# Performance work log

Hardware: AMD Instinct MI355X
Metric: run time of the kernel (lower is better)

Reference implementation:

```python
import jax, jax.numpy as jnp
import numpy as np

B, C, H, W = 4, 32, 128, 256
EPS = 1e-5  # BatchNorm eps


def _conv1x1_bn(x, w, b, gamma, beta, mean, var):
    # x: [B,C,H,W]; 1x1 conv == channel matmul, fused with eval-mode BatchNorm
    y = jnp.einsum('bchw,oc->bohw', x, w) + b[None, :, None, None]
    scale = gamma / jnp.sqrt(var + EPS)
    shift = beta - mean * scale
    return y * scale[None, :, None, None] + shift[None, :, None, None]


def setup_inputs() -> dict:
    key = jax.random.key(0)
    ks = jax.random.split(key, 15)
    d = {
        'x_left': jax.random.normal(ks[0], (B, C, H, W), jnp.float32),
        'x_right': jax.random.normal(ks[1], (B, C, H, W), jnp.float32),
        'cost': jax.random.normal(ks[2], (2, B, H, W, W), jnp.float32),
        'q_w': jax.random.normal(ks[3], (C, C), jnp.float32),
        'q_b': jax.random.normal(ks[4], (C,), jnp.float32),
        'q_gamma': jax.random.uniform(ks[5], (C,), jnp.float32),
        'q_beta': jax.random.normal(ks[6], (C,), jnp.float32),
        'q_mean': jax.random.normal(ks[7], (C,), jnp.float32),
        'q_var': jax.random.uniform(ks[8], (C,), jnp.float32),
        'k_w': jax.random.normal(ks[9], (C, C), jnp.float32),
        'k_b': jax.random.normal(ks[10], (C,), jnp.float32),
        'k_gamma': jax.random.uniform(ks[11], (C,), jnp.float32),
        'k_beta': jax.random.normal(ks[12], (C,), jnp.float32),
        'k_mean': jax.random.normal(ks[13], (C,), jnp.float32),
        'k_var': jax.random.uniform(ks[14], (C,), jnp.float32),
    }
    return d


def reference(x_left, x_right, cost, q_w, q_b, q_gamma, q_beta, q_mean, q_var,
              k_w, k_b, k_gamma, k_beta, k_mean, k_var):
    b, c, h, w = x_left.shape
    cr = w // 3  # clamped_range

    # band masks: right2left keeps 0 <= i-j < cr (lower band); left2right keeps 0 <= j-i < cr
    idx = jnp.arange(w)
    diff = idx[:, None] - idx[None, :]  # [W,W] = i - j
    low_band = ((diff >= 0) & (diff < cr)).astype(x_left.dtype)
    up_band = low_band.T

    # right-to-left: Q from left, K from right
    q_l = jnp.transpose(_conv1x1_bn(x_left, q_w, q_b, q_gamma, q_beta, q_mean, q_var), (0, 2, 3, 1))   # [B,H,W,C]
    k_r = jnp.transpose(_conv1x1_bn(x_right, k_w, k_b, k_gamma, k_beta, k_mean, k_var), (0, 2, 3, 1))  # [B,H,W,C]
    s_r2l = jnp.einsum('bhic,bhjc->bhij', q_l, k_r) / c  # [B,H,W,W]
    cost_r2l = s_r2l * low_band + cost[0]

    # left-to-right: Q from right, K from left
    q_r = jnp.transpose(_conv1x1_bn(x_right, q_w, q_b, q_gamma, q_beta, q_mean, q_var), (0, 2, 3, 1))
    k_l = jnp.transpose(_conv1x1_bn(x_left, k_w, k_b, k_gamma, k_beta, k_mean, k_var), (0, 2, 3, 1))
    s_l2r = jnp.einsum('bhic,bhjc->bhij', q_r, k_l) / c
    cost_l2r = s_l2r * up_band + cost[1]

    # original returns (x_left + fea_left, x_right + fea_right, (r2l, l2r)) with fea == x
    return (x_left * 2.0, x_right * 2.0, cost_r2l, cost_l2r)
```

## Files before the change

kernel.cpp:

```cpp
#include <hip/hip_runtime.h>

#define BB 4
#define CC 32
#define HH 128
#define WW 256
#define CR 85
#define EPSF 1e-5f

#define O1_OFF 4194304
#define O2_OFF 8388608
#define COST1 33554432

typedef __attribute__((ext_vector_type(8))) short bf16x8;
typedef __attribute__((ext_vector_type(4))) float f32x4;
typedef __attribute__((ext_vector_type(4))) float f4v;

#define ARR (512 * 256 * 32)
#define WS_Q(side) ((side) * ARR)
#define WS_K(side) (2 * ARR + (side) * ARR)
#define WS_NEEDED (4ull * ARR * 2ull)

static __device__ __forceinline__ unsigned short f2bf(float f) {
    unsigned u = __float_as_uint(f);
    unsigned r = (u + 0x7FFFu + ((u >> 16) & 1u)) >> 16;
    return (unsigned short)r;
}

__global__ __launch_bounds__(256, 4)
void proj_kernel(const float* __restrict__ x_left, const float* __restrict__ x_right,
                 const float* __restrict__ q_w, const float* __restrict__ q_b,
                 const float* __restrict__ q_gamma, const float* __restrict__ q_beta,
                 const float* __restrict__ q_mean, const float* __restrict__ q_var,
                 const float* __restrict__ k_w, const float* __restrict__ k_b,
                 const float* __restrict__ k_gamma, const float* __restrict__ k_beta,
                 const float* __restrict__ k_mean, const float* __restrict__ k_var,
                 float* __restrict__ out, unsigned short* __restrict__ ws)
{
    __shared__ float wq[CC][CC];
    __shared__ float wk[CC][CC];
    __shared__ float bq[CC], bk[CC], sq[CC], sk[CC];

    const int t    = threadIdx.x;
    const int side = blockIdx.x >> 9;
    const int bh   = blockIdx.x & 511;

    if (t < CC) {
        float qs = q_gamma[t] * rsqrtf(q_var[t] + EPSF);
        float ks = k_gamma[t] * rsqrtf(k_var[t] + EPSF);
        sq[t] = qs; sk[t] = ks;
        bq[t] = q_b[t] * qs + q_beta[t] - q_mean[t] * qs;
        bk[t] = k_b[t] * ks + k_beta[t] - k_mean[t] * ks;
    }
    __syncthreads();
    for (int r = t; r < CC * CC; r += 256) {
        int o = r >> 5, c = r & 31;
        wq[c][o] = q_w[r] * sq[o];
        wk[c][o] = k_w[r] * sk[o];
    }
    __syncthreads();

    float q[CC], k[CC];
    #pragma unroll
    for (int o = 0; o < CC; ++o) { q[o] = bq[o]; k[o] = bk[o]; }

    const float* x = side ? x_right : x_left;
    const int b = bh >> 7, h = bh & 127;
    const int xbase = (b * CC * HH + h) * WW + t;
    float* outx = out + side * O1_OFF;

    #pragma unroll 4
    for (int c = 0; c < CC; ++c) {
        int idx = xbase + c * (HH * WW);
        float xv = __builtin_nontemporal_load(x + idx);
        __builtin_nontemporal_store(2.0f * xv, outx + idx);
        #pragma unroll
        for (int o = 0; o < CC; ++o) {
            q[o] += xv * wq[c][o];
            k[o] += xv * wk[c][o];
        }
    }

    unsigned short* qdst = ws + WS_Q(side) + (bh * WW + t) * CC;
    unsigned short* kdst = ws + WS_K(side) + (bh * WW + t) * CC;
    #pragma unroll
    for (int g = 0; g < 4; ++g) {
        uint4 vq, vk;
        vq.x = f2bf(q[8*g+0]) | ((unsigned)f2bf(q[8*g+1]) << 16);
        vq.y = f2bf(q[8*g+2]) | ((unsigned)f2bf(q[8*g+3]) << 16);
        vq.z = f2bf(q[8*g+4]) | ((unsigned)f2bf(q[8*g+5]) << 16);
        vq.w = f2bf(q[8*g+6]) | ((unsigned)f2bf(q[8*g+7]) << 16);
        vk.x = f2bf(k[8*g+0]) | ((unsigned)f2bf(k[8*g+1]) << 16);
        vk.y = f2bf(k[8*g+2]) | ((unsigned)f2bf(k[8*g+3]) << 16);
        vk.z = f2bf(k[8*g+4]) | ((unsigned)f2bf(k[8*g+5]) << 16);
        vk.w = f2bf(k[8*g+6]) | ((unsigned)f2bf(k[8*g+7]) << 16);
        ((uint4*)qdst)[g] = vq;
        ((uint4*)kdst)[g] = vk;
    }
}

__global__ __launch_bounds__(256, 5)
void score_kernel(const float* __restrict__ cost, const unsigned short* __restrict__ ws,
                  float* __restrict__ out)
{
    __shared__ float Sb[32 * 132];

    const int bx   = (blockIdx.x & 7) * 1024 + (blockIdx.x >> 3);
    const int tile = bx & 7;
    const int bh   = (bx >> 3) & 511;
    const int dir  = bx >> 12;
    const int i0   = tile * 32;
    const int wbase = dir ? i0 : (i0 - 96);

    const unsigned short* qsrc = ws + (dir ? WS_Q(1) : WS_Q(0)) + bh * WW * CC;
    const unsigned short* ksrc = ws + (dir ? WS_K(0) : WS_K(1)) + bh * WW * CC;
    const float* csrc = cost + (size_t)dir * COST1 + (size_t)bh * (WW * WW);
    float* odst = out + O2_OFF + (size_t)dir * COST1 + (size_t)bh * (WW * WW);

    const int t = threadIdx.x;
    const int rowlane = t >> 6;
    const int c4 = 4 * (t & 63);

    f4v vbuf[8];
    #pragma unroll
    for (int p = 0; p < 8; ++p) {
        int rl = 4 * p + rowlane;
        vbuf[p] = __builtin_nontemporal_load((const f4v*)(csrc + (i0 + rl) * WW + c4));
    }

    const int w = t >> 6, lane = t & 63;
    const int quad = lane >> 4, l16 = lane & 15;

    bf16x8 qf[2], kf[2];
    #pragma unroll
    for (int mt = 0; mt < 2; ++mt)
        qf[mt] = *(const bf16x8*)(qsrc + (i0 + 16 * mt + l16) * CC + quad * 8);
    #pragma unroll
    for (int nt = 0; nt < 2; ++nt) {
        int col = wbase + 32 * w + 16 * nt + l16;
        bf16x8 kv = {};
        if (col >= 0 && col < WW)
            kv = *(const bf16x8*)(ksrc + col * CC + quad * 8);
        kf[nt] = kv;
    }

    f32x4 acc[2][2] = {};
    #pragma unroll
    for (int mt = 0; mt < 2; ++mt)
        #pragma unroll
        for (int nt = 0; nt < 2; ++nt)
            acc[mt][nt] = __builtin_amdgcn_mfma_f32_16x16x32_bf16(
                qf[mt], kf[nt], acc[mt][nt], 0, 0, 0);

    #pragma unroll
    for (int mt = 0; mt < 2; ++mt)
        #pragma unroll
        for (int nt = 0; nt < 2; ++nt) {
            int cl = 32 * w + 16 * nt + l16;
            #pragma unroll
            for (int r = 0; r < 4; ++r) {
                int row = 16 * mt + quad * 4 + r;
                Sb[row * 132 + cl] = acc[mt][nt][r];
            }
        }
    __syncthreads();

    const float inv32 = 1.0f / 32.0f;
    const int lc = c4 - wbase;
    const bool inwin = (lc >= 0 && lc < 128);

    #pragma unroll
    for (int p = 0; p < 8; ++p) {
        int rl = 4 * p + rowlane;
        int i = i0 + rl;
        f4v v = vbuf[p];
        if (inwin) {
            const f4v s = *(const f4v*)(Sb + rl * 132 + lc);
            int d0 = dir ? (c4 + 0 - i) : (i - c4 - 0);
            int d1 = dir ? (c4 + 1 - i) : (i - c4 - 1);
            int d2 = dir ? (c4 + 2 - i) : (i - c4 - 2);
            int d3 = dir ? (c4 + 3 - i) : (i - c4 - 3);
            if (d0 >= 0 && d0 < CR) v[0] += s[0] * inv32;
            if (d1 >= 0 && d1 < CR) v[1] += s[1] * inv32;
            if (d2 >= 0 && d2 < CR) v[2] += s[2] * inv32;
            if (d3 >= 0 && d3 < CR) v[3] += s[3] * inv32;
        }
        __builtin_nontemporal_store(v, (f4v*)(odst + (size_t)i * WW + c4));
    }
}

__global__ __launch_bounds__(256, 2)
void pab_fused(const float* __restrict__ x_left, const float* __restrict__ x_right,
               const float* __restrict__ cost,
               const float* __restrict__ q_w, const float* __restrict__ q_b,
               const float* __restrict__ q_gamma, const float* __restrict__ q_beta,
               const float* __restrict__ q_mean, const float* __restrict__ q_var,
               const float* __restrict__ k_w, const float* __restrict__ k_b,
               const float* __restrict__ k_gamma, const float* __restrict__ k_beta,
               const float* __restrict__ k_mean, const float* __restrict__ k_var,
               float* __restrict__ out)
{
    __shared__ float qwt[CC][CC];
    __shared__ float kwt[CC][CC];
    __shared__ float qbf[CC], kbf[CC], qsc[CC], ksc[CC];
    __shared__ float Qls[WW][CC];
    __shared__ float Qrs[WW][CC];

    const int t   = threadIdx.x;
    const int bid = blockIdx.x;
    const int b   = bid >> 7;
    const int h   = bid & 127;

    if (t < CC) {
        float qs = q_gamma[t] * rsqrtf(q_var[t] + EPSF);
        float ks = k_gamma[t] * rsqrtf(k_var[t] + EPSF);
        qsc[t] = qs; ksc[t] = ks;
        qbf[t] = q_b[t] * qs + q_beta[t] - q_mean[t] * qs;
        kbf[t] = k_b[t] * ks + k_beta[t] - k_mean[t] * ks;
    }
    __syncthreads();
    for (int r = t; r < CC * CC; r += 256) {
        int o = r >> 5, c = r & 31;
        qwt[c][o] = q_w[r] * qsc[o];
        kwt[c][o] = k_w[r] * ksc[o];
    }
    __syncthreads();

    float ql[CC], qr[CC], kl[CC], kr[CC];
    #pragma unroll
    for (int o = 0; o < CC; ++o) {
        float qb0 = qbf[o], kb0 = kbf[o];
        ql[o] = qb0; qr[o] = qb0; kl[o] = kb0; kr[o] = kb0;
    }
    const int xbase = (b * CC * HH + h) * WW + t;
    #pragma unroll 4
    for (int c = 0; c < CC; ++c) {
        int idx = xbase + c * (HH * WW);
        float xl = x_left[idx];
        float xr = x_right[idx];
        out[idx]          = 2.0f * xl;
        out[O1_OFF + idx] = 2.0f * xr;
        #pragma unroll
        for (int o = 0; o < CC; ++o) {
            float qw = qwt[c][o];
            float kw = kwt[c][o];
            ql[o] += xl * qw;
            kl[o] += xl * kw;
            qr[o] += xr * qw;
            kr[o] += xr * kw;
        }
    }
    #pragma unroll
    for (int o = 0; o < CC; o += 4) {
        *(float4*)&Qls[t][o] = make_float4(ql[o], ql[o+1], ql[o+2], ql[o+3]);
        *(float4*)&Qrs[t][o] = make_float4(qr[o], qr[o+1], qr[o+2], qr[o+3]);
    }
    __syncthreads();

    const int rowbase = bid * (WW * WW) + t;
    const float* __restrict__ c0 = cost + rowbase;
    const float* __restrict__ c1 = cost + COST1 + rowbase;
    float* __restrict__ o2 = out + O2_OFF + rowbase;
    float* __restrict__ o3 = out + O2_OFF + COST1 + rowbase;

    #pragma unroll 2
    for (int i = 0; i < WW; ++i) {
        float v0 = c0[i * WW];
        float v1 = c1[i * WW];
        int d = i - t;
        if (d >= 0 && d < CR) {
            float s = 0.f;
            #pragma unroll
            for (int o = 0; o < CC; o += 4) {
                float4 q = *(const float4*)&Qls[i][o];
                s += q.x * kr[o] + q.y * kr[o+1] + q.z * kr[o+2] + q.w * kr[o+3];
            }
            v0 += s * (1.0f / 32.0f);
        }
        if (d <= 0 && d > -CR) {
            float s = 0.f;
            #pragma unroll
            for (int o = 0; o < CC; o += 4) {
                float4 q = *(const float4*)&Qrs[i][o];
                s += q.x * kl[o] + q.y * kl[o+1] + q.z * kl[o+2] + q.w * kl[o+3];
            }
            v1 += s * (1.0f / 32.0f);
        }
        o2[i * WW] = v0;
        o3[i * WW] = v1;
    }
}

extern "C" void kernel_launch(void* const* d_in, const int* in_sizes, int n_in,
                              void* d_out, int out_size, void* d_ws, size_t ws_size,
                              hipStream_t stream) {
    const float* x_left  = (const float*)d_in[0];
    const float* x_right = (const float*)d_in[1];
    const float* cost    = (const float*)d_in[2];
    const float* q_w     = (const float*)d_in[3];
    const float* q_b     = (const float*)d_in[4];
    const float* q_gamma = (const float*)d_in[5];
    const float* q_beta  = (const float*)d_in[6];
    const float* q_mean  = (const float*)d_in[7];
    const float* q_var   = (const float*)d_in[8];
    const float* k_w     = (const float*)d_in[9];
    const float* k_b     = (const float*)d_in[10];
    const float* k_gamma = (const float*)d_in[11];
    const float* k_beta  = (const float*)d_in[12];
    const float* k_mean  = (const float*)d_in[13];
    const float* k_var   = (const float*)d_in[14];
    float* out = (float*)d_out;

    if (ws_size >= WS_NEEDED) {
        unsigned short* ws = (unsigned short*)d_ws;
        proj_kernel<<<dim3(1024), dim3(256), 0, stream>>>(
            x_left, x_right,
            q_w, q_b, q_gamma, q_beta, q_mean, q_var,
            k_w, k_b, k_gamma, k_beta, k_mean, k_var,
            out, ws);
        score_kernel<<<dim3(8192), dim3(256), 0, stream>>>(cost, ws, out);
    } else {
        pab_fused<<<dim3(BB * HH), dim3(256), 0, stream>>>(
            x_left, x_right, cost,
            q_w, q_b, q_gamma, q_beta, q_mean, q_var,
            k_w, k_b, k_gamma, k_beta, k_mean, k_var,
            out);
    }
}
```

Measured before the change: 547.3 us.

## Fuse projection and score kernels into one per-row kernel with LDS Q/K

Replaces the separate projection kernel and workspace-based score kernel with a single kernel per (direction, batch, row). It computes bf16 Q and K into shared memory and then loops over eight row tiles doing MFMA scores plus the banded cost add. This removes the workspace write/read and one launch. In exchange it recomputes the projections per direction, reads x twice, and reduces parallelism to 1024 blocks with serial tile loops and extra barriers.

```diff
diff --git a/kernel.cpp b/kernel.cpp
--- a/kernel.cpp
+++ b/kernel.cpp
@@ -15,278 +15,180 @@
 typedef __attribute__((ext_vector_type(4))) float f32x4;
 typedef __attribute__((ext_vector_type(4))) float f4v;
 
-#define ARR (512 * 256 * 32)
-#define WS_Q(side) ((side) * ARR)
-#define WS_K(side) (2 * ARR + (side) * ARR)
-#define WS_NEEDED (4ull * ARR * 2ull)
-
 static __device__ __forceinline__ unsigned short f2bf(float f) {
     unsigned u = __float_as_uint(f);
     unsigned r = (u + 0x7FFFu + ((u >> 16) & 1u)) >> 16;
     return (unsigned short)r;
 }
 
-__global__ __launch_bounds__(256, 4)
-void proj_kernel(const float* __restrict__ x_left, const float* __restrict__ x_right,
-                 const float* __restrict__ q_w, const float* __restrict__ q_b,
-                 const float* __restrict__ q_gamma, const float* __restrict__ q_beta,
-                 const float* __restrict__ q_mean, const float* __restrict__ q_var,
-                 const float* __restrict__ k_w, const float* __restrict__ k_b,
-                 const float* __restrict__ k_gamma, const float* __restrict__ k_beta,
-                 const float* __restrict__ k_mean, const float* __restrict__ k_var,
-                 float* __restrict__ out, unsigned short* __restrict__ ws)
+__global__ __launch_bounds__(256, 3)
+void pab_fused_one(const float* __restrict__ x_left, const float* __restrict__ x_right,
+                   const float* __restrict__ cost,
+                   const float* __restrict__ q_w, const float* __restrict__ q_b,
+                   const float* __restrict__ q_gamma, const float* __restrict__ q_beta,
+                   const float* __restrict__ q_mean, const float* __restrict__ q_var,
+                   const float* __restrict__ k_w, const float* __restrict__ k_b,
+                   const float* __restrict__ k_gamma, const float* __restrict__ k_beta,
+                   const float* __restrict__ k_mean, const float* __restrict__ k_var,
+                   float* __restrict__ out)
 {
-    __shared__ float wq[CC][CC];
-    __shared__ float wk[CC][CC];
-    __shared__ float bq[CC], bk[CC], sq[CC], sk[CC];
-
-    const int t    = threadIdx.x;
-    const int side = blockIdx.x >> 9;
-    const int bh   = blockIdx.x & 511;
+    __shared__ unsigned short Qs[WW * CC];
+    __shared__ unsigned short Ks[WW * CC];
+    __shared__ char smem[32 * 132 * 4];
+    float* Sb = (float*)smem;
+    float (*wqs)[CC] = (float(*)[CC])smem;
+    float (*wks)[CC] = (float(*)[CC])(smem + 4096);
+    float* bqs = (float*)(smem + 8192);
+    float* bks = (float*)(smem + 8320);
+    float* sqs = (float*)(smem + 8448);
+    float* sks = (float*)(smem + 8576);
+
+    const int t   = threadIdx.x;
+    const int dir = blockIdx.x >> 9;
+    const int bh  = blockIdx.x & 511;
+    const int b = bh >> 7, h = bh & 127;
 
     if (t < CC) {
-        float qs = q_gamma[t] * rsqrtf(q_var[t] + EPSF);
-        float ks = k_gamma[t] * rsqrtf(k_var[t] + EPSF);
-        sq[t] = qs; sk[t] = ks;
-        bq[t] = q_b[t] * qs + q_beta[t] - q_mean[t] * qs;
-        bk[t] = k_b[t] * ks + k_beta[t] - k_mean[t] * ks;
+        float qs_ = q_gamma[t] * rsqrtf(q_var[t] + EPSF);
+        float ks_ = k_gamma[t] * rsqrtf(k_var[t] + EPSF);
+        sqs[t] = qs_; sks[t] = ks_;
+        bqs[t] = q_b[t] * qs_ + q_beta[t] - q_mean[t] * qs_;
+        bks[t] = k_b[t] * ks_ + k_beta[t] - k_mean[t] * ks_;
     }
     __syncthreads();
     for (int r = t; r < CC * CC; r += 256) {
         int o = r >> 5, c = r & 31;
-        wq[c][o] = q_w[r] * sq[o];
-        wk[c][o] = k_w[r] * sk[o];
+        wqs[c][o] = q_w[r] * sqs[o];
+        wks[c][o] = k_w[r] * sks[o];
     }
     __syncthreads();
 
-    float q[CC], k[CC];
-    #pragma unroll
-    for (int o = 0; o < CC; ++o) { q[o] = bq[o]; k[o] = bk[o]; }
-
-    const float* x = side ? x_right : x_left;
-    const int b = bh >> 7, h = bh & 127;
+    const float* xq = dir ? x_right : x_left;
+    const float* xk = dir ? x_left  : x_right;
+    float* outq = out + (dir ? O1_OFF : 0);
     const int xbase = (b * CC * HH + h) * WW + t;
-    float* outx = out + side * O1_OFF;
-
-    #pragma unroll 4
-    for (int c = 0; c < CC; ++c) {
-        int idx = xbase + c * (HH * WW);
-        float xv = __builtin_nontemporal_load(x + idx);
-        __builtin_nontemporal_store(2.0f * xv, outx + idx);
-        #pragma unroll
-        for (int o = 0; o < CC; ++o) {
-            q[o] += xv * wq[c][o];
-            k[o] += xv * wk[c][o];
-        }
-    }
-
-    unsigned short* qdst = ws + WS_Q(side) + (bh * WW + t) * CC;
-    unsigned short* kdst = ws + WS_K(side) + (bh * WW + t) * CC;
-    #pragma unroll
-    for (int g = 0; g < 4; ++g) {
-        uint4 vq, vk;
-        vq.x = f2bf(q[8*g+0]) | ((unsigned)f2bf(q[8*g+1]) << 16);
-        vq.y = f2bf(q[8*g+2]) | ((unsigned)f2bf(q[8*g+3]) << 16);
-        vq.z = f2bf(q[8*g+4]) | ((unsigned)f2bf(q[8*g+5]) << 16);
-        vq.w = f2bf(q[8*g+6]) | ((unsigned)f2bf(q[8*g+7]) << 16);
-        vk.x = f2bf(k[8*g+0]) | ((unsigned)f2bf(k[8*g+1]) << 16);
-        vk.y = f2bf(k[8*g+2]) | ((unsigned)f2bf(k[8*g+3]) << 16);
-        vk.z = f2bf(k[8*g+4]) | ((unsigned)f2bf(k[8*g+5]) << 16);
-        vk.w = f2bf(k[8*g+6]) | ((unsigned)f2bf(k[8*g+7]) << 16);
-        ((uint4*)qdst)[g] = vq;
-        ((uint4*)kdst)[g] = vk;
-    }
-}
-
-__global__ __launch_bounds__(256, 5)
-void score_kernel(const float* __restrict__ cost, const unsigned short* __restrict__ ws,
-                  float* __restrict__ out)
-{
-    __shared__ float Sb[32 * 132];
-
-    const int bx   = (blockIdx.x & 7) * 1024 + (blockIdx.x >> 3);
-    const int tile = bx & 7;
-    const int bh   = (bx >> 3) & 511;
-    const int dir  = bx >> 12;
-    const int i0   = tile * 32;
-    const int wbase = dir ? i0 : (i0 - 96);
-
-    const unsigned short* qsrc = ws + (dir ? WS_Q(1) : WS_Q(0)) + bh * WW * CC;
-    const unsigned short* ksrc = ws + (dir ? WS_K(0) : WS_K(1)) + bh * WW * CC;
+
+    {
+        float q[CC];
+        #pragma unroll
+        for (int o = 0; o < CC; ++o) q[o] = bqs[o];
+        #pragma unroll 4
+        for (int c = 0; c < CC; ++c) {
+            int idx = xbase + c * (HH * WW);
+            float xv = xq[idx];
+            __builtin_nontemporal_store(2.0f * xv, outq + idx);
+            #pragma unroll
+            for (int o = 0; o < CC; ++o) q[o] += xv * wqs[c][o];
+        }
+        unsigned short* qdst = Qs + t * CC;
+        #pragma unroll
+        for (int g = 0; g < 4; ++g) {
+            uint4 v;
+            v.x = f2bf(q[8*g+0]) | ((unsigned)f2bf(q[8*g+1]) << 16);
+            v.y = f2bf(q[8*g+2]) | ((unsigned)f2bf(q[8*g+3]) << 16);
+            v.z = f2bf(q[8*g+4]) | ((unsigned)f2bf(q[8*g+5]) << 16);
+            v.w = f2bf(q[8*g+6]) | ((unsigned)f2bf(q[8*g+7]) << 16);
+            ((uint4*)qdst)[g] = v;
+        }
+    }
+    {
+        float k[CC];
+        #pragma unroll
+        for (int o = 0; o < CC; ++o) k[o] = bks[o];
+        #pragma unroll 4
+        for (int c = 0; c < CC; ++c) {
+            float xv = xk[xbase + c * (HH * WW)];
+            #pragma unroll
+            for (int o = 0; o < CC; ++o) k[o] += xv * wks[c][o];
+        }
+        unsigned short* kdst = Ks + t * CC;
+        #pragma unroll
+        for (int g = 0; g < 4; ++g) {
+            uint4 v;
+            v.x = f2bf(k[8*g+0]) | ((unsigned)f2bf(k[8*g+1]) << 16);
+            v.y = f2bf(k[8*g+2]) | ((unsigned)f2bf(k[8*g+3]) << 16);
+            v.z = f2bf(k[8*g+4]) | ((unsigned)f2bf(k[8*g+5]) << 16);
+            v.w = f2bf(k[8*g+6]) | ((unsigned)f2bf(k[8*g+7]) << 16);
+            ((uint4*)kdst)[g] = v;
+        }
+    }
+    __syncthreads();
+
     const float* csrc = cost + (size_t)dir * COST1 + (size_t)bh * (WW * WW);
     float* odst = out + O2_OFF + (size_t)dir * COST1 + (size_t)bh * (WW * WW);
-
-    const int t = threadIdx.x;
     const int rowlane = t >> 6;
     const int c4 = 4 * (t & 63);
-
-    f4v vbuf[8];
-    #pragma unroll
-    for (int p = 0; p < 8; ++p) {
-        int rl = 4 * p + rowlane;
-        vbuf[p] = __builtin_nontemporal_load((const f4v*)(csrc + (i0 + rl) * WW + c4));
-    }
-
     const int w = t >> 6, lane = t & 63;
     const int quad = lane >> 4, l16 = lane & 15;
-
-    bf16x8 qf[2], kf[2];
-    #pragma unroll
-    for (int mt = 0; mt < 2; ++mt)
-        qf[mt] = *(const bf16x8*)(qsrc + (i0 + 16 * mt + l16) * CC + quad * 8);
-    #pragma unroll
-    for (int nt = 0; nt < 2; ++nt) {
-        int col = wbase + 32 * w + 16 * nt + l16;
-        bf16x8 kv = {};
-        if (col >= 0 && col < WW)
-            kv = *(const bf16x8*)(ksrc + col * CC + quad * 8);
-        kf[nt] = kv;
-    }
-
-    f32x4 acc[2][2] = {};
-    #pragma unroll
-    for (int mt = 0; mt < 2; ++mt)
-        #pragma unroll
-        for (int nt = 0; nt < 2; ++nt)
-            acc[mt][nt] = __builtin_amdgcn_mfma_f32_16x16x32_bf16(
-                qf[mt], kf[nt], acc[mt][nt], 0, 0, 0);
-
-    #pragma unroll
-    for (int mt = 0; mt < 2; ++mt)
+    const float inv32 = 1.0f / 32.0f;
+
+    for (int tile = 0; tile < 8; ++tile) {
+        const int i0 = tile * 32;
+        const int wbase = dir ? i0 : (i0 - 96);
+
+        f4v vbuf[8];
+        #pragma unroll
+        for (int p = 0; p < 8; ++p) {
+            int rl = 4 * p + rowlane;
+            vbuf[p] = __builtin_nontemporal_load((const f4v*)(csrc + (i0 + rl) * WW + c4));
+        }
+
+        bf16x8 qf[2], kf[2];
+        #pragma unroll
+        for (int mt = 0; mt < 2; ++mt)
+            qf[mt] = *(const bf16x8*)(Qs + (i0 + 16 * mt + l16) * CC + quad * 8);
         #pragma unroll
         for (int nt = 0; nt < 2; ++nt) {
-            int cl = 32 * w + 16 * nt + l16;
-            #pragma unroll
-            for (int r = 0; r < 4; ++r) {
-                int row = 16 * mt + quad * 4 + r;
-                Sb[row * 132 + cl] = acc[mt][nt][r];
+            int col = wbase + 32 * w + 16 * nt + l16;
+            bf16x8 kv = {};
+            if (col >= 0 && col < WW)
+                kv = *(const bf16x8*)(Ks + col * CC + quad * 8);
+            kf[nt] = kv;
+        }
+
+        f32x4 acc[2][2] = {};
+        #pragma unroll
+        for (int mt = 0; mt < 2; ++mt)
+            #pragma unroll
+            for (int nt = 0; nt < 2; ++nt)
+                acc[mt][nt] = __builtin_amdgcn_mfma_f32_16x16x32_bf16(
+                    qf[mt], kf[nt], acc[mt][nt], 0, 0, 0);
+
+        __syncthreads();
+
+        #pragma unroll
+        for (int mt = 0; mt < 2; ++mt)
+            #pragma unroll
+            for (int nt = 0; nt < 2; ++nt) {
+                int cl = 32 * w + 16 * nt + l16;
+                #pragma unroll
+                for (int r = 0; r < 4; ++r) {
+                    int row = 16 * mt + quad * 4 + r;
+                    Sb[row * 132 + cl] = acc[mt][nt][r];
+                }
             }
-        }
-    __syncthreads();
-
-    const float inv32 = 1.0f / 32.0f;
-    const int lc = c4 - wbase;
-    const bool inwin = (lc >= 0 && lc < 128);
-
-    #pragma unroll
-    for (int p = 0; p < 8; ++p) {
-        int rl = 4 * p + rowlane;
-        int i = i0 + rl;
-        f4v v = vbuf[p];
-        if (inwin) {
-            const f4v s = *(const f4v*)(Sb + rl * 132 + lc);
-            int d0 = dir ? (c4 + 0 - i) : (i - c4 - 0);
-            int d1 = dir ? (c4 + 1 - i) : (i - c4 - 1);
-            int d2 = dir ? (c4 + 2 - i) : (i - c4 - 2);
-            int d3 = dir ? (c4 + 3 - i) : (i - c4 - 3);
-            if (d0 >= 0 && d0 < CR) v[0] += s[0] * inv32;
-            if (d1 >= 0 && d1 < CR) v[1] += s[1] * inv32;
-            if (d2 >= 0 && d2 < CR) v[2] += s[2] * inv32;
-            if (d3 >= 0 && d3 < CR) v[3] += s[3] * inv32;
-        }
-        __builtin_nontemporal_store(v, (f4v*)(odst + (size_t)i * WW + c4));
-    }
-}
-
-__global__ __launch_bounds__(256, 2)
-void pab_fused(const float* __restrict__ x_left, const float* __restrict__ x_right,
-               const float* __restrict__ cost,
-               const float* __restrict__ q_w, const float* __restrict__ q_b,
-               const float* __restrict__ q_gamma, const float* __restrict__ q_beta,
-               const float* __restrict__ q_mean, const float* __restrict__ q_var,
-               const float* __restrict__ k_w, const float* __restrict__ k_b,
-               const float* __restrict__ k_gamma, const float* __restrict__ k_beta,
-               const float* __restrict__ k_mean, const float* __restrict__ k_var,
-               float* __restrict__ out)
-{
-    __shared__ float qwt[CC][CC];
-    __shared__ float kwt[CC][CC];
-    __shared__ float qbf[CC], kbf[CC], qsc[CC], ksc[CC];
-    __shared__ float Qls[WW][CC];
-    __shared__ float Qrs[WW][CC];
-
-    const int t   = threadIdx.x;
-    const int bid = blockIdx.x;
-    const int b   = bid >> 7;
-    const int h   = bid & 127;
-
-    if (t < CC) {
-        float qs = q_gamma[t] * rsqrtf(q_var[t] + EPSF);
-        float ks = k_gamma[t] * rsqrtf(k_var[t] + EPSF);
-        qsc[t] = qs; ksc[t] = ks;
-        qbf[t] = q_b[t] * qs + q_beta[t] - q_mean[t] * qs;
-        kbf[t] = k_b[t] * ks + k_beta[t] - k_mean[t] * ks;
-    }
-    __syncthreads();
-    for (int r = t; r < CC * CC; r += 256) {
-        int o = r >> 5, c = r & 31;
-        qwt[c][o] = q_w[r] * qsc[o];
-        kwt[c][o] = k_w[r] * ksc[o];
-    }
-    __syncthreads();
-
-    float ql[CC], qr[CC], kl[CC], kr[CC];
-    #pragma unroll
-    for (int o = 0; o < CC; ++o) {
-        float qb0 = qbf[o], kb0 = kbf[o];
-        ql[o] = qb0; qr[o] = qb0; kl[o] = kb0; kr[o] = kb0;
-    }
-    const int xbase = (b * CC * HH + h) * WW + t;
-    #pragma unroll 4
-    for (int c = 0; c < CC; ++c) {
-        int idx = xbase + c * (HH * WW);
-        float xl = x_left[idx];
-        float xr = x_right[idx];
-        out[idx]          = 2.0f * xl;
-        out[O1_OFF + idx] = 2.0f * xr;
-        #pragma unroll
-        for (int o = 0; o < CC; ++o) {
-            float qw = qwt[c][o];
-            float kw = kwt[c][o];
-            ql[o] += xl * qw;
-            kl[o] += xl * kw;
-            qr[o] += xr * qw;
-            kr[o] += xr * kw;
-        }
-    }
-    #pragma unroll
-    for (int o = 0; o < CC; o += 4) {
-        *(float4*)&Qls[t][o] = make_float4(ql[o], ql[o+1], ql[o+2], ql[o+3]);
-        *(float4*)&Qrs[t][o] = make_float4(qr[o], qr[o+1], qr[o+2], qr[o+3]);
-    }
-    __syncthreads();
-
-    const int rowbase = bid * (WW * WW) + t;
-    const float* __restrict__ c0 = cost + rowbase;
-    const float* __restrict__ c1 = cost + COST1 + rowbase;
-    float* __restrict__ o2 = out + O2_OFF + rowbase;
-    float* __restrict__ o3 = out + O2_OFF + COST1 + rowbase;
-
-    #pragma unroll 2
-    for (int i = 0; i < WW; ++i) {
-        float v0 = c0[i * WW];
-        float v1 = c1[i * WW];
-        int d = i - t;
-        if (d >= 0 && d < CR) {
-            float s = 0.f;
-            #pragma unroll
-            for (int o = 0; o < CC; o += 4) {
-                float4 q = *(const float4*)&Qls[i][o];
-                s += q.x * kr[o] + q.y * kr[o+1] + q.z * kr[o+2] + q.w * kr[o+3];
+        __syncthreads();
+
+        const int lc = c4 - wbase;
+        const bool inwin = (lc >= 0 && lc < 128);
+        #pragma unroll
+        for (int p = 0; p < 8; ++p) {
+            int rl = 4 * p + rowlane;
+            int i = i0 + rl;
+            f4v v = vbuf[p];
+            if (inwin) {
+                const f4v s = *(const f4v*)(Sb + rl * 132 + lc);
+                int d0 = dir ? (c4 + 0 - i) : (i - c4 - 0);
+                int d1 = dir ? (c4 + 1 - i) : (i - c4 - 1);
+                int d2 = dir ? (c4 + 2 - i) : (i - c4 - 2);
+                int d3 = dir ? (c4 + 3 - i) : (i - c4 - 3);
+                if (d0 >= 0 && d0 < CR) v[0] += s[0] * inv32;
+                if (d1 >= 0 && d1 < CR) v[1] += s[1] * inv32;
+                if (d2 >= 0 && d2 < CR) v[2] += s[2] * inv32;
+                if (d3 >= 0 && d3 < CR) v[3] += s[3] * inv32;
             }
-            v0 += s * (1.0f / 32.0f);
-        }
-        if (d <= 0 && d > -CR) {
-            float s = 0.f;
-            #pragma unroll
-            for (int o = 0; o < CC; o += 4) {
-                float4 q = *(const float4*)&Qrs[i][o];
-                s += q.x * kl[o] + q.y * kl[o+1] + q.z * kl[o+2] + q.w * kl[o+3];
-            }
-            v1 += s * (1.0f / 32.0f);
-        }
-        o2[i * WW] = v0;
-        o3[i * WW] = v1;
+            __builtin_nontemporal_store(v, (f4v*)(odst + (size_t)i * WW + c4));
+        }
     }
 }
 
@@ -310,19 +212,9 @@
     const float* k_var   = (const float*)d_in[14];
     float* out = (float*)d_out;
 
-    if (ws_size >= WS_NEEDED) {
-        unsigned short* ws = (unsigned short*)d_ws;
-        proj_kernel<<<dim3(1024), dim3(256), 0, stream>>>(
-            x_left, x_right,
-            q_w, q_b, q_gamma, q_beta, q_mean, q_var,
-            k_w, k_b, k_gamma, k_beta, k_mean, k_var,
-            out, ws);
-        score_kernel<<<dim3(8192), dim3(256), 0, stream>>>(cost, ws, out);
-    } else {
-        pab_fused<<<dim3(BB * HH), dim3(256), 0, stream>>>(
-            x_left, x_right, cost,
-            q_w, q_b, q_gamma, q_beta, q_mean, q_var,
-            k_w, k_b, k_gamma, k_beta, k_mean, k_var,
-            out);
-    }
+    pab_fused_one<<<dim3(1024), dim3(256), 0, stream>>>(
+        x_left, x_right, cost,
+        q_w, q_b, q_gamma, q_beta, q_mean, q_var,
+        k_w, k_b, k_gamma, k_beta, k_mean, k_var,
+        out);
 }
```

Measured after the change: 531.4 us (median of 2 runs). -2.9%, faster.
